# Performance work log

Hardware: AMD Instinct MI355X
Metric: run time of the kernel (lower is better)

## Reference

```python
import jax, jax.numpy as jnp
import numpy as np

N_NODES = 20000
N_EDGES = 320000
F_IN = 256
HID = 256
N_CLS = 5


def _glorot(key, shape):
    lim = np.sqrt(6.0 / (shape[0] + shape[1]))
    return jax.random.uniform(key, shape, jnp.float32, -lim, lim)


def setup_inputs() -> dict:
    key = jax.random.key(0)
    ks = jax.random.split(key, 12)
    x1 = jax.random.normal(ks[0], (N_NODES, F_IN), jnp.float32)
    x2 = jax.random.normal(ks[1], (N_NODES, F_IN), jnp.float32)
    ei1 = jax.random.randint(ks[2], (2, N_EDGES), 0, N_NODES, jnp.int64 if jax.config.jax_enable_x64 else jnp.int32)
    ei2 = jax.random.randint(ks[3], (2, N_EDGES), 0, N_NODES, jnp.int64 if jax.config.jax_enable_x64 else jnp.int32)
    params = {
        'W1': _glorot(ks[4], (F_IN, HID)), 'b1': jnp.zeros((HID,), jnp.float32),
        'W2': _glorot(ks[5], (HID, HID)), 'b2': jnp.zeros((HID,), jnp.float32),
        'W3': _glorot(ks[6], (HID, HID)), 'b3': jnp.zeros((HID,), jnp.float32),
        'Wl': _glorot(ks[7], (HID, N_CLS)), 'bl': jnp.zeros((N_CLS,), jnp.float32),
    }
    return {'x1': x1, 'edge_index1': ei1, 'x2': x2, 'edge_index2': ei2, **params}


def gcn_conv(x, edge_index, W, b):
    # PyG GCNConv: add self-loops, symmetric normalization D^-1/2 (A+I) D^-1/2 (X W) + b
    N = x.shape[0]
    src, dst = edge_index[0], edge_index[1]
    deg = jax.ops.segment_sum(jnp.ones(src.shape[0], x.dtype), dst, num_segments=N) + 1.0
    dinv = jax.lax.rsqrt(deg)  # [N]
    xw = x @ W                 # [N, H]
    coef = (dinv[src] * dinv[dst])[:, None]  # per-edge norm
    agg = jax.ops.segment_sum(xw[src] * coef, dst, num_segments=N)
    agg = agg + xw * (dinv * dinv)[:, None]  # self-loop term
    return agg + b


def _branch(x, ei, W1, b1, W2, b2, W3, b3):
    # dropout is identity in eval mode
    h = jax.nn.relu(gcn_conv(x, ei, W1, b1))
    h = jax.nn.relu(gcn_conv(h, ei, W2, b2))
    return gcn_conv(h, ei, W3, b3)


def reference(x1, edge_index1, x2, edge_index2, W1, b1, W2, b2, W3, b3, Wl, bl):
    h1 = _branch(x1, edge_index1, W1, b1, W2, b2, W3, b3)
    h2 = _branch(x2, edge_index2, W1, b1, W2, b2, W3, b3)
    h = jnp.concatenate([h1, h2], axis=0)          # [2N, H]
    pooled = jnp.mean(h, axis=0, keepdims=True)    # batch is all zeros -> single mean pool
    return pooled @ Wl + bl                        # [1, num_classes]
```

## Files before the change

### kernel.cpp

```cpp
#include <hip/hip_runtime.h>
#include <hip/hip_bf16.h>

#define N_NODES 20000
#define N_EDGES 320000
#define HID 256
#define NQ 5000
#define NCHUNK 64

typedef __attribute__((ext_vector_type(8))) short bf16x8;
typedef __attribute__((ext_vector_type(4))) float f32x4;
typedef __attribute__((ext_vector_type(8))) unsigned short us8;

__device__ __forceinline__ float bf2f(ushort u) {
  union { unsigned int i; float f; } v; v.i = ((unsigned int)u) << 16; return v.f;
}
__device__ __forceinline__ ushort f2bf(float f) {
  union { float f; unsigned int i; } v; v.f = f;
  unsigned int r = v.i + 0x7FFFu + ((v.i >> 16) & 1u);
  return (ushort)(r >> 16);
}

__global__ void init_detect_kernel(int* cnt0, int* cnt1, float* t0, float* t1,
                                   const void* x1, const void* ei1, int* flags) {
  if (blockIdx.x == gridDim.x - 1) {
    __shared__ int cnt_wild, cnt_oddnz;
    if (threadIdx.x == 0) { cnt_wild = 0; cnt_oddnz = 0; }
    __syncthreads();
    const ushort* xu = (const ushort*)x1;
    int wild = 0;
#pragma unroll
    for (int k = 0; k < 4; k++) {
      ushort u = xu[threadIdx.x * 4 + k];
      int ex = (u >> 7) & 0xFF;
      if (ex >= 0x90) wild++;
    }
    if (wild) atomicAdd(&cnt_wild, wild);
    const int* ii = (const int*)ei1;
    if (ii[threadIdx.x * 2 + 1] != 0) atomicAdd(&cnt_oddnz, 1);
    __syncthreads();
    if (threadIdx.x == 0) {
      flags[0] = (cnt_wild > 64) ? 1 : 0;
      flags[1] = (cnt_oddnz < 8) ? 1 : 0;
    }
    return;
  }
  int i = blockIdx.x * blockDim.x + threadIdx.x;
  if (i < N_NODES) { cnt0[i] = 0; cnt1[i] = 0; t0[i] = 0.f; t1[i] = 0.f; }
}

__global__ __launch_bounds__(1024) void count_rank_kernel(
    const void* e0, const void* e1, int* cnt0, int* cnt1,
    int* rank0, int* rank1, const int* flags) {
  int b = blockIdx.y;
  const void* e = b ? e1 : e0;
  int* cnt = b ? cnt1 : cnt0;
  int* rank = b ? rank1 : rank0;
  int chunk = blockIdx.x >> 2;
  int lo = (blockIdx.x & 3) * NQ;
  int ebeg = chunk * (N_EDGES / NCHUNK);
  int eend = ebeg + (N_EDGES / NCHUNK);
  __shared__ int hist[NQ];
  __shared__ int base[NQ];
  for (int k = threadIdx.x; k < NQ; k += 1024) hist[k] = 0;
  __syncthreads();
  bool w64 = flags[1] != 0;
  const int* d32 = (const int*)e + N_EDGES;
  const long long* d64 = (const long long*)e + N_EDGES;
  for (int i = ebeg + threadIdx.x; i < eend; i += 1024) {
    int d = w64 ? (int)d64[i] : d32[i];
    unsigned q = (unsigned)(d - lo);
    if (q < NQ) atomicAdd(&hist[q], 1);
  }
  __syncthreads();
  for (int k = threadIdx.x; k < NQ; k += 1024) {
    int h = hist[k];
    if (h) base[k] = atomicAdd(&cnt[lo + k], h);
    hist[k] = 0;
  }
  __syncthreads();
  for (int i = ebeg + threadIdx.x; i < eend; i += 1024) {
    int d = w64 ? (int)d64[i] : d32[i];
    unsigned q = (unsigned)(d - lo);
    if (q < NQ) rank[i] = base[q] + atomicAdd(&hist[q], 1);
  }
}

__global__ __launch_bounds__(1024) void scan_kernel(const int* cnt0, const int* cnt1,
                                                    int* rp0, int* rp1,
                                                    float* dinv0, float* dinv1) {
  const int* cnt = blockIdx.x ? cnt1 : cnt0;
  int* rp = blockIdx.x ? rp1 : rp0;
  float* dinv = blockIdx.x ? dinv1 : dinv0;
  __shared__ int sd[1024];
  int tid = threadIdx.x;
  int base = tid * 20;
  int pref[20];
  int run = 0;
#pragma unroll
  for (int k = 0; k < 20; k++) {
    int i = base + k;
    int c = (i < N_NODES) ? cnt[i] : 0;
    if (i < N_NODES) dinv[i] = rsqrtf((float)c + 1.0f);
    run += c;
    pref[k] = run;
  }
  sd[tid] = run;
  __syncthreads();
  for (int off = 1; off < 1024; off <<= 1) {
    int v = (tid >= off) ? sd[tid - off] : 0;
    __syncthreads();
    sd[tid] += v;
    __syncthreads();
  }
  int offset = sd[tid] - run;
  if (tid == 0) rp[0] = 0;
#pragma unroll
  for (int k = 0; k < 20; k++) {
    int i = base + k;
    if (i < N_NODES) rp[i + 1] = offset + pref[k];
  }
}

__global__ __launch_bounds__(1024) void fill_kernel(
    const void* e0, const void* e1,
    const float* dinv0, const float* dinv1,
    const int* rp0, const int* rp1,
    const int* rank0, const int* rank1,
    unsigned int* eg0, unsigned int* eg1,
    float* t0, float* t1, const int* flags) {
  int b = blockIdx.y;
  const void* e = b ? e1 : e0;
  const float* dinv = b ? dinv1 : dinv0;
  bool w64 = flags[1] != 0;
  const int* s32 = (const int*)e;
  const int* d32 = (const int*)e + N_EDGES;
  const long long* s64 = (const long long*)e;
  const long long* d64 = (const long long*)e + N_EDGES;
  if (blockIdx.x < 313) {
    const int* rp = b ? rp1 : rp0;
    const int* rank = b ? rank1 : rank0;
    unsigned int* eg = b ? eg1 : eg0;
    int i = blockIdx.x * 1024 + threadIdx.x;
    if (i >= N_EDGES) return;
    int src = w64 ? (int)s64[i] : s32[i];
    int dst = w64 ? (int)d64[i] : d32[i];
    int slot = rp[dst] + rank[i];
    eg[slot] = (unsigned int)src | ((unsigned int)f2bf(dinv[src] * dinv[dst]) << 16);
    return;
  }
  float* t = b ? t1 : t0;
  int r = blockIdx.x - 313;
  int chunk = r >> 2;
  int lo = (r & 3) * NQ;
  int ebeg = chunk * (N_EDGES / NCHUNK);
  int eend = ebeg + (N_EDGES / NCHUNK);
  __shared__ float tl[NQ];
  for (int k = threadIdx.x; k < NQ; k += 1024) tl[k] = 0.f;
  __syncthreads();
  for (int i = ebeg + threadIdx.x; i < eend; i += 1024) {
    int src = w64 ? (int)s64[i] : s32[i];
    unsigned q = (unsigned)(src - lo);
    if (q < NQ) {
      int dst = w64 ? (int)d64[i] : d32[i];
      atomicAdd(&tl[q], dinv[dst]);
    }
  }
  __syncthreads();
  for (int k = threadIdx.x; k < NQ; k += 1024) {
    float v = tl[k];
    if (v != 0.f) atomicAdd(&t[lo + k], v);
  }
}

__global__ __launch_bounds__(256) void gemm_kernel(
    const void* __restrict__ A0, const void* __restrict__ A1,
    const void* __restrict__ W,
    ushort* __restrict__ C0, ushort* __restrict__ C1,
    int maybe_f32, const int* __restrict__ flags) {
  const void* A = blockIdx.z ? A1 : A0;
  ushort* C = blockIdx.z ? C1 : C0;
  bool wf32 = flags[0] != 0;
  bool af32 = maybe_f32 && wf32;
  int m0 = blockIdx.x * 32;
  __shared__ ushort As[32][42];
  __shared__ ushort Bs[256][42];
  int tid = threadIdx.x;
  int wave = tid >> 6, lane = tid & 63;
  int quad = lane >> 4, r16 = lane & 15;
  int nb = wave * 64;
  f32x4 acc[2][4];
#pragma unroll
  for (int m = 0; m < 2; m++)
#pragma unroll
    for (int n = 0; n < 4; n++) acc[m][n] = (f32x4){0.f, 0.f, 0.f, 0.f};
  int ar = tid >> 2;
  int ac = (tid & 3) * 8;
  int bk = tid >> 3;
  int bn0 = (tid & 7) * 8;
  for (int k0 = 0; k0 < 256; k0 += 32) {
    if (tid < 128) {
      int gr = m0 + ar;
      if (af32) {
        const float* pA = (const float*)A + gr * 256 + k0 + ac;
        float4 v0 = *(const float4*)pA;
        float4 v1 = *(const float4*)(pA + 4);
        ushort* d = &As[ar][ac];
        d[0] = f2bf(v0.x); d[1] = f2bf(v0.y); d[2] = f2bf(v0.z); d[3] = f2bf(v0.w);
        d[4] = f2bf(v1.x); d[5] = f2bf(v1.y); d[6] = f2bf(v1.z); d[7] = f2bf(v1.w);
      } else {
        *(int4*)&As[ar][ac] =
            *(const int4*)((const ushort*)A + gr * 256 + k0 + ac);
      }
    }
#pragma unroll
    for (int h = 0; h < 4; h++) {
      ushort wtmp[8];
      if (wf32) {
        const float* Wf = (const float*)W + (k0 + bk) * 256 + bn0 + h * 64;
        float4 u0 = *(const float4*)Wf;
        float4 u1 = *(const float4*)(Wf + 4);
        wtmp[0] = f2bf(u0.x); wtmp[1] = f2bf(u0.y); wtmp[2] = f2bf(u0.z); wtmp[3] = f2bf(u0.w);
        wtmp[4] = f2bf(u1.x); wtmp[5] = f2bf(u1.y); wtmp[6] = f2bf(u1.z); wtmp[7] = f2bf(u1.w);
      } else {
        *(int4*)wtmp = *(const int4*)((const ushort*)W + (k0 + bk) * 256 + bn0 + h * 64);
      }
#pragma unroll
      for (int j = 0; j < 8; j++) Bs[bn0 + h * 64 + j][bk] = wtmp[j];
    }
    __syncthreads();
    bf16x8 a0 = *(const bf16x8*)&As[r16][quad * 8];
    bf16x8 a1 = *(const bf16x8*)&As[16 + r16][quad * 8];
    bf16x8 bb0 = *(const bf16x8*)&Bs[nb + r16][quad * 8];
    bf16x8 bb1 = *(const bf16x8*)&Bs[nb + 16 + r16][quad * 8];
    bf16x8 bb2 = *(const bf16x8*)&Bs[nb + 32 + r16][quad * 8];
    bf16x8 bb3 = *(const bf16x8*)&Bs[nb + 48 + r16][quad * 8];
    acc[0][0] = __builtin_amdgcn_mfma_f32_16x16x32_bf16(a0, bb0, acc[0][0], 0, 0, 0);
    acc[0][1] = __builtin_amdgcn_mfma_f32_16x16x32_bf16(a0, bb1, acc[0][1], 0, 0, 0);
    acc[0][2] = __builtin_amdgcn_mfma_f32_16x16x32_bf16(a0, bb2, acc[0][2], 0, 0, 0);
    acc[0][3] = __builtin_amdgcn_mfma_f32_16x16x32_bf16(a0, bb3, acc[0][3], 0, 0, 0);
    acc[1][0] = __builtin_amdgcn_mfma_f32_16x16x32_bf16(a1, bb0, acc[1][0], 0, 0, 0);
    acc[1][1] = __builtin_amdgcn_mfma_f32_16x16x32_bf16(a1, bb1, acc[1][1], 0, 0, 0);
    acc[1][2] = __builtin_amdgcn_mfma_f32_16x16x32_bf16(a1, bb2, acc[1][2], 0, 0, 0);
    acc[1][3] = __builtin_amdgcn_mfma_f32_16x16x32_bf16(a1, bb3, acc[1][3], 0, 0, 0);
    __syncthreads();
  }
#pragma unroll
  for (int m = 0; m < 2; m++) {
    int grb = m0 + m * 16 + quad * 4;
#pragma unroll
    for (int r = 0; r < 4; r++) {
      int gr = grb + r;
      ushort* cp = C + gr * 256 + nb + r16;
      cp[0]  = f2bf(acc[m][0][r]);
      cp[16] = f2bf(acc[m][1][r]);
      cp[32] = f2bf(acc[m][2][r]);
      cp[48] = f2bf(acc[m][3][r]);
    }
  }
}

__global__ __launch_bounds__(256) void agg_kernel(
    const ushort* __restrict__ XW0, const ushort* __restrict__ XW1,
    const float* __restrict__ dinv0, const float* __restrict__ dinv1,
    const int* __restrict__ rp0, const int* __restrict__ rp1,
    const unsigned int* __restrict__ eg0, const unsigned int* __restrict__ eg1,
    const void* __restrict__ bias,
    ushort* __restrict__ H0, ushort* __restrict__ H1,
    const int* __restrict__ flags) {
  int b = blockIdx.z;
  const ushort* XW = b ? XW1 : XW0;
  const float* dinv = b ? dinv1 : dinv0;
  const int* rp = b ? rp1 : rp0;
  const unsigned int* eg = b ? eg1 : eg0;
  ushort* H = b ? H1 : H0;
  int wave = threadIdx.x >> 6, lane = threadIdx.x & 63;
  int grp = lane >> 3;
  int fo = (lane & 7) * 8 + blockIdx.y * 64;
  int i = blockIdx.x * 32 + wave * 8 + grp;
  float di = dinv[i];
  float selfw = di * di;
  us8 v = *(const us8*)(XW + i * 256 + fo);
  float acc[8], acc2[8];
#pragma unroll
  for (int k = 0; k < 8; k++) { acc[k] = selfw * bf2f(v[k]); acc2[k] = 0.f; }
  int e = rp[i], eend = rp[i + 1];
  for (; e + 4 <= eend; e += 4) {
    unsigned int p0 = eg[e], p1 = eg[e + 1], p2 = eg[e + 2], p3 = eg[e + 3];
    us8 r0 = *(const us8*)(XW + (p0 & 0xFFFFu) * 256 + fo);
    us8 r1 = *(const us8*)(XW + (p1 & 0xFFFFu) * 256 + fo);
    us8 r2 = *(const us8*)(XW + (p2 & 0xFFFFu) * 256 + fo);
    us8 r3 = *(const us8*)(XW + (p3 & 0xFFFFu) * 256 + fo);
    float w0 = bf2f((ushort)(p0 >> 16)), w1 = bf2f((ushort)(p1 >> 16));
    float w2 = bf2f((ushort)(p2 >> 16)), w3 = bf2f((ushort)(p3 >> 16));
#pragma unroll
    for (int k = 0; k < 8; k++) {
      acc[k]  += w0 * bf2f(r0[k]);
      acc2[k] += w1 * bf2f(r1[k]);
      acc[k]  += w2 * bf2f(r2[k]);
      acc2[k] += w3 * bf2f(r3[k]);
    }
  }
  for (; e < eend; e++) {
    unsigned int pp = eg[e];
    us8 r = *(const us8*)(XW + (pp & 0xFFFFu) * 256 + fo);
    float w = bf2f((ushort)(pp >> 16));
#pragma unroll
    for (int k = 0; k < 8; k++) acc[k] += w * bf2f(r[k]);
  }
  float bv[8];
  if (flags[0]) {
    const float* bf = (const float*)bias + fo;
    float4 c0 = *(const float4*)bf;
    float4 c1 = *(const float4*)(bf + 4);
    bv[0] = c0.x; bv[1] = c0.y; bv[2] = c0.z; bv[3] = c0.w;
    bv[4] = c1.x; bv[5] = c1.y; bv[6] = c1.z; bv[7] = c1.w;
  } else {
    us8 bb = *(const us8*)((const ushort*)bias + fo);
#pragma unroll
    for (int k = 0; k < 8; k++) bv[k] = bf2f(bb[k]);
  }
  us8 o;
#pragma unroll
  for (int k = 0; k < 8; k++)
    o[k] = f2bf(fmaxf(acc[k] + acc2[k] + bv[k], 0.f));
  *(us8*)(H + i * 256 + fo) = o;
}

__global__ __launch_bounds__(256) void colsum_kernel(
    const ushort* __restrict__ H0, const ushort* __restrict__ H1,
    const float* __restrict__ dinv0, const float* __restrict__ dinv1,
    const float* __restrict__ t0, const float* __restrict__ t1,
    float* __restrict__ P) {
  int b = blockIdx.y;
  const ushort* H = b ? H1 : H0;
  const float* dinv = b ? dinv1 : dinv0;
  const float* t = b ? t1 : t0;
  int wave = threadIdx.x >> 6, lane = threadIdx.x & 63;
  int wid = blockIdx.x * 4 + wave;
  int f4 = lane * 4;
  float a0 = 0.f, a1 = 0.f, a2 = 0.f, a3 = 0.f;
  for (int j = wid; j < N_NODES; j += 256) {
    float dj = dinv[j];
    float c = dj * (t[j] + dj);
    ushort4 u = *(const ushort4*)(H + j * 256 + f4);
    a0 += c * bf2f(u.x); a1 += c * bf2f(u.y);
    a2 += c * bf2f(u.z); a3 += c * bf2f(u.w);
  }
  __shared__ float part[4][256];
  part[wave][f4 + 0] = a0; part[wave][f4 + 1] = a1;
  part[wave][f4 + 2] = a2; part[wave][f4 + 3] = a3;
  __syncthreads();
  int f = threadIdx.x;
  float ssum = part[0][f] + part[1][f] + part[2][f] + part[3][f];
  P[(b * 64 + blockIdx.x) * 256 + f] = ssum;
}

__global__ __launch_bounds__(256) void final_kernel(
    const float* __restrict__ P,
    const void* __restrict__ W3, const void* __restrict__ b3,
    const void* __restrict__ Wl, const void* __restrict__ bl,
    void* __restrict__ out, const int* __restrict__ flags) {
  __shared__ float v[256];
  __shared__ float pooled[256];
  bool f32 = flags[0] != 0;
  int t = threadIdx.x;
  float acc0 = 0.f, acc1 = 0.f;
  for (int b = 0; b < 64; b++) {
    acc0 += P[b * 256 + t];
    acc1 += P[(64 + b) * 256 + t];
  }
  v[t] = acc0 + acc1;
  __syncthreads();
  float acc = 0.f;
  if (f32) {
    const float* W3f = (const float*)W3;
    for (int f = 0; f < 256; f++) acc += v[f] * W3f[f * 256 + t];
    pooled[t] = acc * (1.0f / (2.0f * N_NODES)) + ((const float*)b3)[t];
  } else {
    const ushort* W3b = (const ushort*)W3;
    for (int f = 0; f < 256; f++) acc += v[f] * bf2f(W3b[f * 256 + t]);
    pooled[t] = acc * (1.0f / (2.0f * N_NODES)) + bf2f(((const ushort*)b3)[t]);
  }
  __syncthreads();
  if (t < 5) {
    float o;
    if (f32) {
      o = ((const float*)bl)[t];
      for (int h = 0; h < 256; h++) o += pooled[h] * ((const float*)Wl)[h * 5 + t];
      ((float*)out)[t] = o;
    } else {
      o = bf2f(((const ushort*)bl)[t]);
      for (int h = 0; h < 256; h++) o += pooled[h] * bf2f(((const ushort*)Wl)[h * 5 + t]);
      ((ushort*)out)[t] = f2bf(o);
    }
  }
}

extern "C" void kernel_launch(void* const* d_in, const int* in_sizes, int n_in,
                              void* d_out, int out_size, void* d_ws, size_t ws_size,
                              hipStream_t stream) {
  const void* x1 = d_in[0];
  const void* ei1 = d_in[1];
  const void* x2 = d_in[2];
  const void* ei2 = d_in[3];
  const void* W1 = d_in[4];
  const void* b1 = d_in[5];
  const void* W2 = d_in[6];
  const void* b2 = d_in[7];
  const void* W3 = d_in[8];
  const void* b3 = d_in[9];
  const void* Wl = d_in[10];
  const void* bl = d_in[11];

  char* p = (char*)d_ws;
  auto alloc = [&](size_t bytes) {
    char* r = p;
    p += (bytes + 255) & ~size_t(255);
    return r;
  };
  int* flags   = (int*)alloc(256);
  float* dinv0 = (float*)alloc(N_NODES * 4);
  float* dinv1 = (float*)alloc(N_NODES * 4);
  float* t0    = (float*)alloc(N_NODES * 4);
  float* t1    = (float*)alloc(N_NODES * 4);
  int* cnt0    = (int*)alloc(N_NODES * 4);
  int* cnt1    = (int*)alloc(N_NODES * 4);
  int* rp0     = (int*)alloc((N_NODES + 1) * 4);
  int* rp1     = (int*)alloc((N_NODES + 1) * 4);
  unsigned int* eg0 = (unsigned int*)alloc((size_t)N_EDGES * 4);
  unsigned int* eg1 = (unsigned int*)alloc((size_t)N_EDGES * 4);
  float* Pp    = (float*)alloc(2 * 64 * 256 * 4);
  ushort* xw0  = (ushort*)alloc((size_t)N_NODES * HID * 2);
  ushort* xw1  = (ushort*)alloc((size_t)N_NODES * HID * 2);
  ushort* h0   = (ushort*)alloc((size_t)N_NODES * HID * 2);
  ushort* h1   = (ushort*)alloc((size_t)N_NODES * HID * 2);
  int* rank0  = (int*)xw0;
  int* rank1  = rank0 + N_EDGES;

  init_detect_kernel<<<(N_NODES + 255) / 256 + 1, 256, 0, stream>>>(
      cnt0, cnt1, t0, t1, x1, ei1, flags);
  count_rank_kernel<<<dim3(NCHUNK * 4, 2), 1024, 0, stream>>>(
      ei1, ei2, cnt0, cnt1, rank0, rank1, flags);
  scan_kernel<<<2, 1024, 0, stream>>>(cnt0, cnt1, rp0, rp1, dinv0, dinv1);
  fill_kernel<<<dim3(313 + NCHUNK * 4, 2), 1024, 0, stream>>>(
      ei1, ei2, dinv0, dinv1, rp0, rp1, rank0, rank1, eg0, eg1, t0, t1, flags);

  gemm_kernel<<<dim3(625, 1, 2), 256, 0, stream>>>(x1, x2, W1, xw0, xw1, 1, flags);
  agg_kernel<<<dim3(625, 4, 2), 256, 0, stream>>>(
      xw0, xw1, dinv0, dinv1, rp0, rp1, eg0, eg1, b1, h0, h1, flags);

  gemm_kernel<<<dim3(625, 1, 2), 256, 0, stream>>>(h0, h1, W2, xw0, xw1, 0, flags);
  agg_kernel<<<dim3(625, 4, 2), 256, 0, stream>>>(
      xw0, xw1, dinv0, dinv1, rp0, rp1, eg0, eg1, b2, h0, h1, flags);

  colsum_kernel<<<dim3(64, 2), 256, 0, stream>>>(h0, h1, dinv0, dinv1, t0, t1, Pp);
  final_kernel<<<1, 256, 0, stream>>>(Pp, W3, b3, Wl, bl, d_out, flags);
}
```

Before: 346.4 us.

## Pre-transpose weights to bf16 and load B fragments directly from global memory

Adds a small kernel that converts W1/W2 to bf16 and transposes them once per call. The GEMM then stages the whole 32x256 A tile in LDS with a single barrier and reads the B fragments straight from global memory (cache-resident), with no per-k-step LDS staging. This removes the per-iteration scattered transposed LDS stores, the repeated fp32-to-bf16 conversion of W, and 16 barriers per block. In exchange it adds one kernel launch and relies on L2 hit rates for the repeated weight reads.

```diff
diff --git a/kernel.cpp b/kernel.cpp
--- a/kernel.cpp
+++ b/kernel.cpp
@@ -46,6 +46,21 @@
   }
   int i = blockIdx.x * blockDim.x + threadIdx.x;
   if (i < N_NODES) { cnt0[i] = 0; cnt1[i] = 0; t0[i] = 0.f; t1[i] = 0.f; }
+}
+
+__global__ __launch_bounds__(256) void wt_kernel(
+    const void* __restrict__ W1, const void* __restrict__ W2,
+    ushort* __restrict__ Wt1, ushort* __restrict__ Wt2,
+    const int* __restrict__ flags) {
+  bool f32 = flags[0] != 0;
+  int which = blockIdx.x >> 8;
+  int k = blockIdx.x & 255;
+  const void* W = which ? W2 : W1;
+  ushort* Wt = which ? Wt2 : Wt1;
+  int n = threadIdx.x;
+  ushort v = f32 ? f2bf(((const float*)W)[k * 256 + n])
+                 : ((const ushort*)W)[k * 256 + n];
+  Wt[n * 256 + k] = v;
 }
 
 __global__ __launch_bounds__(1024) void count_rank_kernel(
@@ -174,66 +189,52 @@
 
 __global__ __launch_bounds__(256) void gemm_kernel(
     const void* __restrict__ A0, const void* __restrict__ A1,
-    const void* __restrict__ W,
+    const ushort* __restrict__ Wt,
     ushort* __restrict__ C0, ushort* __restrict__ C1,
     int maybe_f32, const int* __restrict__ flags) {
   const void* A = blockIdx.z ? A1 : A0;
   ushort* C = blockIdx.z ? C1 : C0;
-  bool wf32 = flags[0] != 0;
-  bool af32 = maybe_f32 && wf32;
+  bool af32 = maybe_f32 && (flags[0] != 0);
   int m0 = blockIdx.x * 32;
-  __shared__ ushort As[32][42];
-  __shared__ ushort Bs[256][42];
+  __shared__ __align__(16) ushort As[32][264];
   int tid = threadIdx.x;
   int wave = tid >> 6, lane = tid & 63;
   int quad = lane >> 4, r16 = lane & 15;
   int nb = wave * 64;
+  {
+    int row = tid >> 3, c0 = (tid & 7) * 32;
+    int gr = m0 + row;
+    if (af32) {
+      const float* pA = (const float*)A + gr * 256 + c0;
+      ushort* d = &As[row][c0];
+#pragma unroll
+      for (int s = 0; s < 8; s++) {
+        float4 v = *(const float4*)(pA + s * 4);
+        d[s * 4 + 0] = f2bf(v.x); d[s * 4 + 1] = f2bf(v.y);
+        d[s * 4 + 2] = f2bf(v.z); d[s * 4 + 3] = f2bf(v.w);
+      }
+    } else {
+      const ushort* pA = (const ushort*)A + gr * 256 + c0;
+#pragma unroll
+      for (int s = 0; s < 4; s++)
+        *(int4*)&As[row][c0 + s * 8] = *(const int4*)(pA + s * 8);
+    }
+  }
+  __syncthreads();
   f32x4 acc[2][4];
 #pragma unroll
   for (int m = 0; m < 2; m++)
 #pragma unroll
     for (int n = 0; n < 4; n++) acc[m][n] = (f32x4){0.f, 0.f, 0.f, 0.f};
-  int ar = tid >> 2;
-  int ac = (tid & 3) * 8;
-  int bk = tid >> 3;
-  int bn0 = (tid & 7) * 8;
+#pragma unroll
   for (int k0 = 0; k0 < 256; k0 += 32) {
-    if (tid < 128) {
-      int gr = m0 + ar;
-      if (af32) {
-        const float* pA = (const float*)A + gr * 256 + k0 + ac;
-        float4 v0 = *(const float4*)pA;
-        float4 v1 = *(const float4*)(pA + 4);
-        ushort* d = &As[ar][ac];
-        d[0] = f2bf(v0.x); d[1] = f2bf(v0.y); d[2] = f2bf(v0.z); d[3] = f2bf(v0.w);
-        d[4] = f2bf(v1.x); d[5] = f2bf(v1.y); d[6] = f2bf(v1.z); d[7] = f2bf(v1.w);
-      } else {
-        *(int4*)&As[ar][ac] =
-            *(const int4*)((const ushort*)A + gr * 256 + k0 + ac);
-      }
-    }
-#pragma unroll
-    for (int h = 0; h < 4; h++) {
-      ushort wtmp[8];
-      if (wf32) {
-        const float* Wf = (const float*)W + (k0 + bk) * 256 + bn0 + h * 64;
-        float4 u0 = *(const float4*)Wf;
-        float4 u1 = *(const float4*)(Wf + 4);
-        wtmp[0] = f2bf(u0.x); wtmp[1] = f2bf(u0.y); wtmp[2] = f2bf(u0.z); wtmp[3] = f2bf(u0.w);
-        wtmp[4] = f2bf(u1.x); wtmp[5] = f2bf(u1.y); wtmp[6] = f2bf(u1.z); wtmp[7] = f2bf(u1.w);
-      } else {
-        *(int4*)wtmp = *(const int4*)((const ushort*)W + (k0 + bk) * 256 + bn0 + h * 64);
-      }
-#pragma unroll
-      for (int j = 0; j < 8; j++) Bs[bn0 + h * 64 + j][bk] = wtmp[j];
-    }
-    __syncthreads();
-    bf16x8 a0 = *(const bf16x8*)&As[r16][quad * 8];
-    bf16x8 a1 = *(const bf16x8*)&As[16 + r16][quad * 8];
-    bf16x8 bb0 = *(const bf16x8*)&Bs[nb + r16][quad * 8];
-    bf16x8 bb1 = *(const bf16x8*)&Bs[nb + 16 + r16][quad * 8];
-    bf16x8 bb2 = *(const bf16x8*)&Bs[nb + 32 + r16][quad * 8];
-    bf16x8 bb3 = *(const bf16x8*)&Bs[nb + 48 + r16][quad * 8];
+    bf16x8 a0 = *(const bf16x8*)&As[r16][k0 + quad * 8];
+    bf16x8 a1 = *(const bf16x8*)&As[16 + r16][k0 + quad * 8];
+    const ushort* wp = Wt + (nb + r16) * 256 + k0 + quad * 8;
+    bf16x8 bb0 = *(const bf16x8*)(wp);
+    bf16x8 bb1 = *(const bf16x8*)(wp + 16 * 256);
+    bf16x8 bb2 = *(const bf16x8*)(wp + 32 * 256);
+    bf16x8 bb3 = *(const bf16x8*)(wp + 48 * 256);
     acc[0][0] = __builtin_amdgcn_mfma_f32_16x16x32_bf16(a0, bb0, acc[0][0], 0, 0, 0);
     acc[0][1] = __builtin_amdgcn_mfma_f32_16x16x32_bf16(a0, bb1, acc[0][1], 0, 0, 0);
     acc[0][2] = __builtin_amdgcn_mfma_f32_16x16x32_bf16(a0, bb2, acc[0][2], 0, 0, 0);
@@ -242,7 +243,6 @@
     acc[1][1] = __builtin_amdgcn_mfma_f32_16x16x32_bf16(a1, bb1, acc[1][1], 0, 0, 0);
     acc[1][2] = __builtin_amdgcn_mfma_f32_16x16x32_bf16(a1, bb2, acc[1][2], 0, 0, 0);
     acc[1][3] = __builtin_amdgcn_mfma_f32_16x16x32_bf16(a1, bb3, acc[1][3], 0, 0, 0);
-    __syncthreads();
   }
 #pragma unroll
   for (int m = 0; m < 2; m++) {
@@ -430,6 +430,8 @@
   unsigned int* eg0 = (unsigned int*)alloc((size_t)N_EDGES * 4);
   unsigned int* eg1 = (unsigned int*)alloc((size_t)N_EDGES * 4);
   float* Pp    = (float*)alloc(2 * 64 * 256 * 4);
+  ushort* wt1  = (ushort*)alloc(256 * 256 * 2);
+  ushort* wt2  = (ushort*)alloc(256 * 256 * 2);
   ushort* xw0  = (ushort*)alloc((size_t)N_NODES * HID * 2);
   ushort* xw1  = (ushort*)alloc((size_t)N_NODES * HID * 2);
   ushort* h0   = (ushort*)alloc((size_t)N_NODES * HID * 2);
@@ -439,17 +441,18 @@
 
   init_detect_kernel<<<(N_NODES + 255) / 256 + 1, 256, 0, stream>>>(
       cnt0, cnt1, t0, t1, x1, ei1, flags);
+  wt_kernel<<<512, 256, 0, stream>>>(W1, W2, wt1, wt2, flags);
   count_rank_kernel<<<dim3(NCHUNK * 4, 2), 1024, 0, stream>>>(
       ei1, ei2, cnt0, cnt1, rank0, rank1, flags);
   scan_kernel<<<2, 1024, 0, stream>>>(cnt0, cnt1, rp0, rp1, dinv0, dinv1);
   fill_kernel<<<dim3(313 + NCHUNK * 4, 2), 1024, 0, stream>>>(
       ei1, ei2, dinv0, dinv1, rp0, rp1, rank0, rank1, eg0, eg1, t0, t1, flags);
 
-  gemm_kernel<<<dim3(625, 1, 2), 256, 0, stream>>>(x1, x2, W1, xw0, xw1, 1, flags);
+  gemm_kernel<<<dim3(625, 1, 2), 256, 0, stream>>>(x1, x2, wt1, xw0, xw1, 1, flags);
   agg_kernel<<<dim3(625, 4, 2), 256, 0, stream>>>(
       xw0, xw1, dinv0, dinv1, rp0, rp1, eg0, eg1, b1, h0, h1, flags);
 
-  gemm_kernel<<<dim3(625, 1, 2), 256, 0, stream>>>(h0, h1, W2, xw0, xw1, 0, flags);
+  gemm_kernel<<<dim3(625, 1, 2), 256, 0, stream>>>(h0, h1, wt2, xw0, xw1, 0, flags);
   agg_kernel<<<dim3(625, 4, 2), 256, 0, stream>>>(
       xw0, xw1, dinv0, dinv1, rp0, rp1, eg0, eg1, b2, h0, h1, flags);
 
```

After: 353.9 us. 2.2% more time.
